# Kernel optimization log

Hardware: AMD Instinct MI355X
Metric: run time of the kernel (lower is better)

## Reference

```python
import jax, jax.numpy as jnp
import numpy as np

NEG_INF = -1e9
LRELU_SLOPE = 0.2


def setup_inputs() -> dict:
    N, F_IN, F_OUT = 8192, 256, 128
    key = jax.random.key(0)
    k_adj, k_x, k_w, k_phi = jax.random.split(key, 4)
    adj = (jax.random.uniform(k_adj, (N, N)) < 0.01).astype(jnp.float32)
    x = jax.random.normal(k_x, (N, F_IN), dtype=jnp.float32)
    stdv_w = 1.0 / np.sqrt(F_OUT)
    weight = jax.random.uniform(k_w, (F_IN, F_OUT), minval=-stdv_w, maxval=stdv_w, dtype=jnp.float32)
    bias = jnp.zeros((F_OUT,), dtype=jnp.float32)
    phi = jax.random.uniform(k_phi, (2 * F_OUT, 1), minval=-1.0, maxval=1.0, dtype=jnp.float32)
    return {"adj": adj, "input": x, "weight": weight, "bias": bias, "phi": phi}


def reference(adj, input, weight, bias, phi):
    # x_prime: [N, F_OUT]
    x_prime = input @ weight + bias
    N = adj.shape[0]
    F_out = x_prime.shape[1]
    # S[i, j] = cat(x_i, x_j) @ phi = x_i @ phi[:F] + x_j @ phi[F:]
    # (identical math to the repeat+cat formulation, without the O(N^2*2F) tensor)
    phi_src = phi[:F_out, 0]  # [F_OUT]
    phi_dst = phi[F_out:, 0]  # [F_OUT]
    s_src = x_prime @ phi_src  # [N]
    s_dst = x_prime @ phi_dst  # [N]
    S = s_src[:, None] + s_dst[None, :]  # [N, N]
    S = jnp.where(S >= 0, S, LRELU_SLOPE * S)  # leaky_relu(0.2)
    mask = (adj + jnp.eye(N, dtype=adj.dtype)) > 0
    S_masked = jnp.where(mask, S, NEG_INF)
    attention = jax.nn.softmax(S_masked, axis=1)  # row-wise
    h = attention @ x_prime  # [N, F_OUT]
    return h
```

## Files before the change

kernel.cpp:

```cpp
#include <hip/hip_runtime.h>

#define Nn    8192
#define FIN   256
#define FOUTc 128
#define MAXN  512

typedef float f32x4 __attribute__((ext_vector_type(4)));

__global__ __launch_bounds__(256) void k_prep(const float* __restrict__ w,
                                              const float* __restrict__ phi,
                                              float* __restrict__ wps,
                                              float* __restrict__ wpd)
{
    const int k    = blockIdx.x * 4 + (threadIdx.x >> 6);
    const int lane = threadIdx.x & 63;
    const float2 wv = ((const float2*)(w + (size_t)k * FOUTc))[lane];
    const float2 ps = ((const float2*)phi)[lane];
    const float2 pd = ((const float2*)(phi + FOUTc))[lane];
    float a = wv.x * ps.x + wv.y * ps.y;
    float b = wv.x * pd.x + wv.y * pd.y;
#pragma unroll
    for (int off = 32; off > 0; off >>= 1) {
        a += __shfl_down(a, off, 64);
        b += __shfl_down(b, off, 64);
    }
    if (lane == 0) { wps[k] = a; wpd[k] = b; }
}

__global__ __launch_bounds__(256) void k_s(const float* __restrict__ x,
                                           const float* __restrict__ wps,
                                           const float* __restrict__ wpd,
                                           float* __restrict__ s_src,
                                           float* __restrict__ s_dst)
{
    const int wid = threadIdx.x >> 6, lane = threadIdx.x & 63;
    const int row = blockIdx.x * 4 + wid;
    const float* xr = x + (size_t)row * FIN;
    float a = 0.f, b = 0.f;
#pragma unroll
    for (int q = 0; q < 4; q++) {
        const int k = lane + 64 * q;
        const float xv = xr[k];
        a = fmaf(xv, wps[k], a);
        b = fmaf(xv, wpd[k], b);
    }
#pragma unroll
    for (int off = 32; off > 0; off >>= 1) {
        a += __shfl_down(a, off, 64);
        b += __shfl_down(b, off, 64);
    }
    if (lane == 0) { s_src[row] = a; s_dst[row] = b; }
}

__global__ __launch_bounds__(512) void k_agg(const float* __restrict__ adj,
                                             const float* __restrict__ x,
                                             const float* __restrict__ w,
                                             const float* __restrict__ bias,
                                             const float* __restrict__ s_src,
                                             const float* __restrict__ s_dst,
                                             float* __restrict__ out)
{
    __shared__ int   nbr[MAXN];
    __shared__ float wts[MAXN];
    __shared__ float zs2[2][FIN];
    __shared__ float ph[4][FOUTc];
    __shared__ float red[8];
    __shared__ int   cnt;

    const int tid = threadIdx.x;
    const int i = blockIdx.x;
    if (tid == 0) cnt = 0;
    __syncthreads();

    const f32x4* arow4 = (const f32x4*)(adj + (size_t)i * Nn);
    f32x4 buf[4];
#pragma unroll
    for (int t = 0; t < 4; t++) buf[t] = __builtin_nontemporal_load(arow4 + t * 512 + tid);

#pragma unroll
    for (int t = 0; t < 4; t++) {
        const int j0 = (t * 512 + tid) * 4;
#pragma unroll
        for (int p = 0; p < 4; p++) {
            const int j = j0 + p;
            if (buf[t][p] != 0.f || j == i) {
                const int pos = atomicAdd(&cnt, 1);
                if (pos < MAXN) nbr[pos] = j;
            }
        }
    }
    __syncthreads();
    const int L    = (cnt < MAXN) ? cnt : MAXN;
    const int Lpad = (L + 7) & ~7;
    if (tid < Lpad - L) nbr[L + tid] = i;

    float lmax = -1e30f;
    for (int n = tid; n < L; n += 512) {
        const float sd = s_dst[nbr[n]];
        wts[n] = sd;
        lmax = fmaxf(lmax, sd);
    }
#pragma unroll
    for (int off = 32; off > 0; off >>= 1) lmax = fmaxf(lmax, __shfl_down(lmax, off, 64));
    if ((tid & 63) == 0) red[tid >> 6] = lmax;
    __syncthreads();
    float maxd = red[0];
#pragma unroll
    for (int r = 1; r < 8; r++) maxd = fmaxf(maxd, red[r]);
    const float ssi = s_src[i];
    const float Sm  = ssi + maxd;
    const float m_i = (Sm >= 0.f) ? Sm : 0.2f * Sm;

    float lsum = 0.f;
    for (int n = tid; n < L; n += 512) {
        float S = ssi + wts[n];
        S = (S >= 0.f) ? S : 0.2f * S;
        const float wv = __expf(S - m_i);
        wts[n] = wv;
        lsum += wv;
    }
    if (tid < Lpad - L) wts[L + tid] = 0.f;
#pragma unroll
    for (int off = 32; off > 0; off >>= 1) lsum += __shfl_down(lsum, off, 64);
    __syncthreads();
    if ((tid & 63) == 0) red[tid >> 6] = lsum;
    __syncthreads();
    float l_i = red[0];
#pragma unroll
    for (int r = 1; r < 8; r++) l_i += red[r];
    const float inv = 1.f / l_i;

    const int c = tid & 255;
    const int g = tid >> 8;
    const int Lh = Lpad >> 1;
    const int base = g * Lh;
    const float* xc = x + c;
    float z0 = 0.f, z1 = 0.f, z2 = 0.f, z3 = 0.f;
    for (int n = base; n < base + Lh; n += 4) {
        const int j0 = nbr[n], j1 = nbr[n+1], j2 = nbr[n+2], j3 = nbr[n+3];
        const float w0 = wts[n], w1 = wts[n+1], w2 = wts[n+2], w3 = wts[n+3];
        z0 = fmaf(w0, xc[(size_t)j0 * FIN], z0);
        z1 = fmaf(w1, xc[(size_t)j1 * FIN], z1);
        z2 = fmaf(w2, xc[(size_t)j2 * FIN], z2);
        z3 = fmaf(w3, xc[(size_t)j3 * FIN], z3);
    }
    zs2[g][c] = (z0 + z1) + (z2 + z3);
    __syncthreads();

    const int o = tid & 127, q = tid >> 7;
    const float* wcol = w + (size_t)(q * 64) * FOUTc + o;
    float acc = 0.f;
#pragma unroll 8
    for (int k = 0; k < 64; k++) {
        const float zsum = zs2[0][q * 64 + k] + zs2[1][q * 64 + k];
        acc = fmaf(zsum, wcol[(size_t)k * FOUTc], acc);
    }
    ph[q][o] = acc;
    __syncthreads();
    if (tid < FOUTc)
        out[(size_t)i * FOUTc + tid] =
            (ph[0][tid] + ph[1][tid] + ph[2][tid] + ph[3][tid]) * inv + bias[tid];
}

extern "C" void kernel_launch(void* const* d_in, const int* in_sizes, int n_in,
                              void* d_out, int out_size, void* d_ws, size_t ws_size,
                              hipStream_t stream)
{
    (void)out_size; (void)ws_size;
    const float* adj  = (const float*)d_in[0];
    const float* x    = (const float*)d_in[1];
    const float* w    = (const float*)d_in[2];
    const float* bias = (const float*)d_in[3];
    const float* phi  = (const float*)d_in[4];
    for (int i = 0; i < n_in; i++) {
        switch (in_sizes[i]) {
            case Nn * Nn:     adj  = (const float*)d_in[i]; break;
            case Nn * FIN:    x    = (const float*)d_in[i]; break;
            case FIN * FOUTc: w    = (const float*)d_in[i]; break;
            case FOUTc:       bias = (const float*)d_in[i]; break;
            case 2 * FOUTc:   phi  = (const float*)d_in[i]; break;
        }
    }
    float* out = (float*)d_out;

    float* wps   = (float*)d_ws;
    float* wpd   = wps + FIN;
    float* s_src = wpd + FIN;
    float* s_dst = s_src + Nn;

    hipLaunchKernelGGL(k_prep, dim3(64),   dim3(256), 0, stream, w, phi, wps, wpd);
    hipLaunchKernelGGL(k_s,    dim3(Nn/4), dim3(256), 0, stream, x, wps, wpd, s_src, s_dst);
    hipLaunchKernelGGL(k_agg,  dim3(Nn),   dim3(512), 0, stream,
                       adj, x, w, bias, s_src, s_dst, out);
}
```

Before: 425.4 us.

## Precompute projected features once and gather from them in aggregation

Replaces the per-row gather over 256-wide input features followed by a per-row 256x128 weight product with a separate kernel that first computes x' = xW + b for all nodes along with the source and destination scores. The aggregation kernel then gathers 128-wide projected rows, which halves gather traffic and removes the redundant per-row matrix-vector product. In exchange it adds a 4 MB intermediate write and read, and the projection kernel uses plain scalar FMAs with 512 blocks, so it may itself be slow.

```diff
diff --git a/kernel.cpp b/kernel.cpp
--- a/kernel.cpp
+++ b/kernel.cpp
@@ -7,63 +7,64 @@
 
 typedef float f32x4 __attribute__((ext_vector_type(4)));
 
-__global__ __launch_bounds__(256) void k_prep(const float* __restrict__ w,
-                                              const float* __restrict__ phi,
-                                              float* __restrict__ wps,
-                                              float* __restrict__ wpd)
+__global__ __launch_bounds__(256) void k_xp(const float* __restrict__ x,
+                                            const float* __restrict__ w,
+                                            const float* __restrict__ bias,
+                                            const float* __restrict__ phi,
+                                            float* __restrict__ xp,
+                                            float* __restrict__ s_src,
+                                            float* __restrict__ s_dst)
 {
-    const int k    = blockIdx.x * 4 + (threadIdx.x >> 6);
+    const int wave = blockIdx.x * 4 + (threadIdx.x >> 6);
     const int lane = threadIdx.x & 63;
-    const float2 wv = ((const float2*)(w + (size_t)k * FOUTc))[lane];
+    const int row0 = wave * 4;
+
+    const float2 bv = ((const float2*)bias)[lane];
     const float2 ps = ((const float2*)phi)[lane];
     const float2 pd = ((const float2*)(phi + FOUTc))[lane];
-    float a = wv.x * ps.x + wv.y * ps.y;
-    float b = wv.x * pd.x + wv.y * pd.y;
+
+    const float* xr = x + (size_t)row0 * FIN;
+    float2 acc[4];
 #pragma unroll
-    for (int off = 32; off > 0; off >>= 1) {
-        a += __shfl_down(a, off, 64);
-        b += __shfl_down(b, off, 64);
+    for (int r = 0; r < 4; r++) acc[r] = make_float2(0.f, 0.f);
+
+#pragma unroll 4
+    for (int k = 0; k < FIN; k++) {
+        const float2 wv = ((const float2*)(w + (size_t)k * FOUTc))[lane];
+        const float xv0 = xr[k];
+        const float xv1 = xr[FIN + k];
+        const float xv2 = xr[2 * FIN + k];
+        const float xv3 = xr[3 * FIN + k];
+        acc[0].x = fmaf(xv0, wv.x, acc[0].x); acc[0].y = fmaf(xv0, wv.y, acc[0].y);
+        acc[1].x = fmaf(xv1, wv.x, acc[1].x); acc[1].y = fmaf(xv1, wv.y, acc[1].y);
+        acc[2].x = fmaf(xv2, wv.x, acc[2].x); acc[2].y = fmaf(xv2, wv.y, acc[2].y);
+        acc[3].x = fmaf(xv3, wv.x, acc[3].x); acc[3].y = fmaf(xv3, wv.y, acc[3].y);
     }
-    if (lane == 0) { wps[k] = a; wpd[k] = b; }
-}
 
-__global__ __launch_bounds__(256) void k_s(const float* __restrict__ x,
-                                           const float* __restrict__ wps,
-                                           const float* __restrict__ wpd,
-                                           float* __restrict__ s_src,
-                                           float* __restrict__ s_dst)
-{
-    const int wid = threadIdx.x >> 6, lane = threadIdx.x & 63;
-    const int row = blockIdx.x * 4 + wid;
-    const float* xr = x + (size_t)row * FIN;
-    float a = 0.f, b = 0.f;
 #pragma unroll
-    for (int q = 0; q < 4; q++) {
-        const int k = lane + 64 * q;
-        const float xv = xr[k];
-        a = fmaf(xv, wps[k], a);
-        b = fmaf(xv, wpd[k], b);
+    for (int r = 0; r < 4; r++) {
+        const float2 h = make_float2(acc[r].x + bv.x, acc[r].y + bv.y);
+        ((float2*)(xp + (size_t)(row0 + r) * FOUTc))[lane] = h;
+        float a = h.x * ps.x + h.y * ps.y;
+        float b = h.x * pd.x + h.y * pd.y;
+#pragma unroll
+        for (int off = 32; off > 0; off >>= 1) {
+            a += __shfl_down(a, off, 64);
+            b += __shfl_down(b, off, 64);
+        }
+        if (lane == 0) { s_src[row0 + r] = a; s_dst[row0 + r] = b; }
     }
-#pragma unroll
-    for (int off = 32; off > 0; off >>= 1) {
-        a += __shfl_down(a, off, 64);
-        b += __shfl_down(b, off, 64);
-    }
-    if (lane == 0) { s_src[row] = a; s_dst[row] = b; }
 }
 
 __global__ __launch_bounds__(512) void k_agg(const float* __restrict__ adj,
-                                             const float* __restrict__ x,
-                                             const float* __restrict__ w,
-                                             const float* __restrict__ bias,
+                                             const float* __restrict__ xp,
                                              const float* __restrict__ s_src,
                                              const float* __restrict__ s_dst,
                                              float* __restrict__ out)
 {
     __shared__ int   nbr[MAXN];
     __shared__ float wts[MAXN];
-    __shared__ float zs2[2][FIN];
-    __shared__ float ph[4][FOUTc];
+    __shared__ float hp[4][FOUTc];
     __shared__ float red[8];
     __shared__ int   cnt;
 
@@ -130,36 +131,23 @@
     for (int r = 1; r < 8; r++) l_i += red[r];
     const float inv = 1.f / l_i;
 
-    const int c = tid & 255;
-    const int g = tid >> 8;
-    const int Lh = Lpad >> 1;
-    const int base = g * Lh;
-    const float* xc = x + c;
-    float z0 = 0.f, z1 = 0.f, z2 = 0.f, z3 = 0.f;
-    for (int n = base; n < base + Lh; n += 4) {
-        const int j0 = nbr[n], j1 = nbr[n+1], j2 = nbr[n+2], j3 = nbr[n+3];
-        const float w0 = wts[n], w1 = wts[n+1], w2 = wts[n+2], w3 = wts[n+3];
-        z0 = fmaf(w0, xc[(size_t)j0 * FIN], z0);
-        z1 = fmaf(w1, xc[(size_t)j1 * FIN], z1);
-        z2 = fmaf(w2, xc[(size_t)j2 * FIN], z2);
-        z3 = fmaf(w3, xc[(size_t)j3 * FIN], z3);
+    const int o  = tid & 127;
+    const int g  = tid >> 7;
+    const int Lq = Lpad >> 2;
+    const int base = g * Lq;
+    const float* xpo = xp + o;
+    float h0 = 0.f, h1 = 0.f;
+    for (int n = base; n < base + Lq; n += 2) {
+        const int   j0 = nbr[n],   j1 = nbr[n + 1];
+        const float w0 = wts[n],   w1 = wts[n + 1];
+        h0 = fmaf(w0, xpo[(size_t)j0 * FOUTc], h0);
+        h1 = fmaf(w1, xpo[(size_t)j1 * FOUTc], h1);
     }
-    zs2[g][c] = (z0 + z1) + (z2 + z3);
-    __syncthreads();
-
-    const int o = tid & 127, q = tid >> 7;
-    const float* wcol = w + (size_t)(q * 64) * FOUTc + o;
-    float acc = 0.f;
-#pragma unroll 8
-    for (int k = 0; k < 64; k++) {
-        const float zsum = zs2[0][q * 64 + k] + zs2[1][q * 64 + k];
-        acc = fmaf(zsum, wcol[(size_t)k * FOUTc], acc);
-    }
-    ph[q][o] = acc;
+    hp[g][o] = h0 + h1;
     __syncthreads();
     if (tid < FOUTc)
         out[(size_t)i * FOUTc + tid] =
-            (ph[0][tid] + ph[1][tid] + ph[2][tid] + ph[3][tid]) * inv + bias[tid];
+            ((hp[0][tid] + hp[1][tid]) + (hp[2][tid] + hp[3][tid])) * inv;
 }
 
 extern "C" void kernel_launch(void* const* d_in, const int* in_sizes, int n_in,
@@ -183,13 +171,12 @@
     }
     float* out = (float*)d_out;
 
-    float* wps   = (float*)d_ws;
-    float* wpd   = wps + FIN;
-    float* s_src = wpd + FIN;
+    float* xp    = (float*)d_ws;
+    float* s_src = xp + (size_t)Nn * FOUTc;
     float* s_dst = s_src + Nn;
 
-    hipLaunchKernelGGL(k_prep, dim3(64),   dim3(256), 0, stream, w, phi, wps, wpd);
-    hipLaunchKernelGGL(k_s,    dim3(Nn/4), dim3(256), 0, stream, x, wps, wpd, s_src, s_dst);
-    hipLaunchKernelGGL(k_agg,  dim3(Nn),   dim3(512), 0, stream,
-                       adj, x, w, bias, s_src, s_dst, out);
+    hipLaunchKernelGGL(k_xp,  dim3(512), dim3(256), 0, stream,
+                       x, w, bias, phi, xp, s_src, s_dst);
+    hipLaunchKernelGGL(k_agg, dim3(Nn),  dim3(512), 0, stream,
+                       adj, xp, s_src, s_dst, out);
 }
```

Result: faster. 409.1 us (-3.8%).
